# Performance work log

Hardware: AMD Instinct MI355X
Metric: run time of the kernel (lower is better)

## Reference

```python
import jax, jax.numpy as jnp
from jax import lax
import numpy as np

B, T, E, H, V = 64, 512, 256, 256, 50000

def _lstm_dir(xs, Wih, Whh, b, reverse):
    # xs: [T, B, in_dim]; PyTorch gate order i,f,g,o; returns (outputs [T,B,H], final h [B,H])
    def step(carry, xt):
        h, c = carry
        g = xt @ Wih.T + h @ Whh.T + b
        i, f, gg, o = jnp.split(g, 4, axis=-1)
        c = jax.nn.sigmoid(f) * c + jax.nn.sigmoid(i) * jnp.tanh(gg)
        h = jax.nn.sigmoid(o) * jnp.tanh(c)
        return (h, c), h
    z = jnp.zeros((xs.shape[1], Whh.shape[1]), xs.dtype)
    (hT, _), hs = lax.scan(step, (z, z), xs, reverse=reverse)
    return hs, hT

def setup_inputs() -> dict:
    key = jax.random.key(0)
    ks = jax.random.split(key, 20)
    s = 1.0 / np.sqrt(H)
    u = lambda k, sh: jax.random.uniform(k, sh, jnp.float32, -s, s)
    x = jax.random.randint(ks[0], (B, T), 0, V)
    embed = jax.random.normal(ks[1], (V, E), jnp.float32)
    embed = embed.at[0].set(0.0)  # padding_idx=0
    d = {"x": x, "embed": embed}
    i = 2
    for l, in_dim in [(0, E), (1, 2 * H)]:
        for dname in ("f", "b"):
            d[f"Wih_l{l}_{dname}"] = u(ks[i], (4 * H, in_dim)); i += 1
            d[f"Whh_l{l}_{dname}"] = u(ks[i], (4 * H, H)); i += 1
            d[f"b_l{l}_{dname}"] = u(ks[i], (4 * H,)); i += 1  # = b_ih + b_hh fused
    d["Wlin"] = u(ks[i], (1, 2 * H)); d["blin"] = u(ks[i + 1], (1,))
    return d

def reference(x, embed, Wih_l0_f, Whh_l0_f, b_l0_f, Wih_l0_b, Whh_l0_b, b_l0_b,
              Wih_l1_f, Whh_l1_f, b_l1_f, Wih_l1_b, Whh_l1_b, b_l1_b, Wlin, blin):
    xs = embed[x].transpose(1, 0, 2)  # [T, B, E]
    # layer 0
    hf, _ = _lstm_dir(xs, Wih_l0_f, Whh_l0_f, b_l0_f, reverse=False)
    hb, _ = _lstm_dir(xs, Wih_l0_b, Whh_l0_b, b_l0_b, reverse=True)
    xs1 = jnp.concatenate([hf, hb], axis=-1)  # [T, B, 2H]
    # layer 1
    _, hTf = _lstm_dir(xs1, Wih_l1_f, Whh_l1_f, b_l1_f, reverse=False)
    _, hTb = _lstm_dir(xs1, Wih_l1_b, Whh_l1_b, b_l1_b, reverse=True)
    last = jnp.concatenate([hTf, hTb], axis=-1)  # [B, 2H]
    out = last @ Wlin.T + blin  # [B, 1]
    return out[:, 0]
```

## Files before the change

kernel.cpp:

```cpp
#include <hip/hip_runtime.h>
#include <hip/hip_fp16.h>


typedef _Float16 f16;
typedef _Float16 half8 __attribute__((ext_vector_type(8)));
typedef float floatx4 __attribute__((ext_vector_type(4)));

#if __has_builtin(__builtin_amdgcn_global_load_lds)
#define HAS_GLL 1
#endif

#if __has_builtin(__builtin_amdgcn_exp2f)
#define EXP2F __builtin_amdgcn_exp2f
#else
#define EXP2F exp2f
#endif
#if __has_builtin(__builtin_amdgcn_rcpf)
#define RCPF __builtin_amdgcn_rcpf
#else
#define RCPF(x) (1.0f/(x))
#endif

__device__ __forceinline__ float sigf(float x) {
  return RCPF(1.f + EXP2F(-1.4426950408889634f * x));
}
__device__ __forceinline__ float tanhf_(float x) {
  return 2.f * RCPF(1.f + EXP2F(-2.8853900817779268f * x)) - 1.f;
}


__global__ void k_cvt_embed(const float* __restrict__ src, f16* __restrict__ dst, int n8) {
  int i = blockIdx.x * blockDim.x + threadIdx.x;
  if (i >= n8) return;
  const float4* s = (const float4*)(src + (size_t)i * 8);
  float4 a = s[0], b = s[1];
  half8 h = { (f16)a.x,(f16)a.y,(f16)a.z,(f16)a.w,(f16)b.x,(f16)b.y,(f16)b.z,(f16)b.w };
  *(half8*)(dst + (size_t)i * 8) = h;
}

__global__ void k_cvt_wih(const float* __restrict__ sf, const float* __restrict__ sb,
                          f16* __restrict__ dst, int K, int logK, int total) {
  int i = blockIdx.x * blockDim.x + threadIdx.x;
  if (i >= total) return;
  int k = i & (K - 1);
  int n = i >> logK;
  int d = n >> 10;
  int rem = n & 1023;
  int j = rem >> 2, g = rem & 3;
  const float* s = d ? sb : sf;
  dst[i] = (f16)s[(size_t)((g << 8) + j) * K + k];
}

__global__ void k_cvt_whh(const float* __restrict__ sf, const float* __restrict__ sb,
                          f16* __restrict__ dst) {
  int i = blockIdx.x * blockDim.x + threadIdx.x;
  if (i >= 524288) return;
  int d = i >> 18, rem = i & 262143;
  dst[i] = (f16)((d ? sb : sf)[rem]);
}


template<int KD, bool GATHER>
__global__ __launch_bounds__(256)
void k_gemm(const f16* __restrict__ Abase, const f16* __restrict__ Bmat,
            const int* __restrict__ xtok, f16* __restrict__ C) {
  __shared__ __align__(16) char Al[128 * 64 * 2];
  __shared__ __align__(16) char Bl[128 * 64 * 2];
  __shared__ int toks[128];
  const int tid = threadIdx.x;
  const int lane = tid & 63, wave = tid >> 6;
  const int mt = blockIdx.x & 255;
  const int nt = blockIdx.x >> 8;
  const int Mb = mt * 128, Nb = nt * 128;

  if (GATHER) {
    if (tid < 128) {
      int m = Mb + tid;
      toks[tid] = xtok[(m & 63) * 512 + (m >> 6)];
    }
  }
  __syncthreads();

  const f16* asrc[4]; const f16* bsrc[4];
#pragma unroll
  for (int it = 0; it < 4; ++it) {
    int g = it * 256 + tid;
    int row = g >> 3, gc = g & 7;
    if (GATHER) asrc[it] = Abase + (size_t)toks[row] * KD + gc * 8;
    else        asrc[it] = Abase + (size_t)(Mb + row) * KD + gc * 8;
    bsrc[it] = Bmat + (size_t)(Nb + row) * KD + gc * 8;
  }

  floatx4 acc[4][4];
#pragma unroll
  for (int mi = 0; mi < 4; ++mi)
#pragma unroll
    for (int ni = 0; ni < 4; ++ni)
      acc[mi][ni] = (floatx4){0.f, 0.f, 0.f, 0.f};

  const int wr = wave >> 1, wc = wave & 1;

  for (int kt = 0; kt < KD / 64; ++kt) {
    __syncthreads();
#ifdef HAS_GLL
#pragma unroll
    for (int it = 0; it < 4; ++it) {
      __builtin_amdgcn_global_load_lds(
          (const __attribute__((address_space(1))) void*)(asrc[it]),
          (__attribute__((address_space(3))) void*)(Al + (it * 256 + wave * 64) * 16), 16, 0, 0);
      __builtin_amdgcn_global_load_lds(
          (const __attribute__((address_space(1))) void*)(bsrc[it]),
          (__attribute__((address_space(3))) void*)(Bl + (it * 256 + wave * 64) * 16), 16, 0, 0);
      asrc[it] += 64; bsrc[it] += 64;
    }
#else
    uint4 va[4], vb[4];
#pragma unroll
    for (int it = 0; it < 4; ++it) {
      va[it] = *(const uint4*)(asrc[it]);
      vb[it] = *(const uint4*)(bsrc[it]);
      asrc[it] += 64; bsrc[it] += 64;
    }
#pragma unroll
    for (int it = 0; it < 4; ++it) {
      *(uint4*)(Al + (it * 256 + wave * 64) * 16 + lane * 16) = va[it];
      *(uint4*)(Bl + (it * 256 + wave * 64) * 16 + lane * 16) = vb[it];
    }
#endif
    __syncthreads();

#pragma unroll
    for (int kk = 0; kk < 2; ++kk) {
      half8 av[4], bv[4];
#pragma unroll
      for (int mi = 0; mi < 4; ++mi) {
        int row = wr * 64 + mi * 16 + (lane & 15);
        av[mi] = *(const half8*)(Al + row * 128 + kk * 64 + (lane >> 4) * 16);
      }
#pragma unroll
      for (int ni = 0; ni < 4; ++ni) {
        int row = wc * 64 + ni * 16 + (lane & 15);
        bv[ni] = *(const half8*)(Bl + row * 128 + kk * 64 + (lane >> 4) * 16);
      }
#pragma unroll
      for (int mi = 0; mi < 4; ++mi)
#pragma unroll
        for (int ni = 0; ni < 4; ++ni)
          acc[mi][ni] = __builtin_amdgcn_mfma_f32_16x16x32_f16(av[mi], bv[ni], acc[mi][ni], 0, 0, 0);
    }
  }

#pragma unroll
  for (int mi = 0; mi < 4; ++mi) {
#pragma unroll
    for (int ni = 0; ni < 4; ++ni) {
      floatx4 v = acc[mi][ni];
      int n = Nb + wc * 64 + ni * 16 + (lane & 15);
#pragma unroll
      for (int r = 0; r < 4; ++r) {
        int m = Mb + wr * 64 + mi * 16 + (lane >> 4) * 4 + r;
        C[(size_t)m * 2048 + n] = (f16)v[r];
      }
    }
  }
}


template<int LAYER, int OWNBASE>
__device__ __forceinline__ void scan_body(
    const f16* __restrict__ proj, const f16* __restrict__ whh,
    const float* __restrict__ bias_f, const float* __restrict__ bias_b,
    f16* ring, float* __restrict__ finalh, unsigned* __restrict__ ctr,
    char* Hl) {
  constexpr int PEERBASE = 128 - OWNBASE;
  constexpr int BLK = OWNBASE >> 7;
  const int tid = threadIdx.x, lane = tid & 63, wave = tid >> 6;
  const int gid = blockIdx.x & 7;
  const int d = gid & 1, bgrp = gid >> 1;
  const int bbase = bgrp * 16;
  const int rowsel = lane >> 4, l15 = lane & 15;
  const int jlocal = OWNBASE + wave * 16 + l15;
  const int klocal = wave * 16 + l15;
  const int bA = l15;
  unsigned* flagOwn  = ctr + gid * 64 + BLK * 16;
  unsigned* flagPeer = ctr + gid * 64 + (1 - BLK) * 16;

  half8 wreg[4][8];
#pragma unroll
  for (int g = 0; g < 4; ++g)
#pragma unroll
    for (int kk = 0; kk < 8; ++kk)
      wreg[g][kk] = *(const half8*)(whh + ((size_t)(d * 1024 + g * 256 + jlocal)) * 256
                                    + kk * 32 + rowsel * 8);

  const float* bptr = d ? bias_b : bias_f;
  float bias[4];
#pragma unroll
  for (int g = 0; g < 4; ++g) bias[g] = bptr[g * 256 + jlocal];

  *(uint4*)(Hl + tid * 16) = make_uint4(0, 0, 0, 0);
  {
    const int gslot = d ? 513 : 0;
    int zr = tid >> 5, zc = (tid & 31) * 4;
    *(uint2*)(ring + ((size_t)gslot * 64 + bbase + zr) * 512 + d * 256 + OWNBASE + zc) =
        make_uint2(0, 0);
  }
  __syncthreads();
  if (tid == 0)
    __hip_atomic_store(flagOwn, 1u, __ATOMIC_RELEASE, __HIP_MEMORY_SCOPE_AGENT);

  float cst[4] = {0.f, 0.f, 0.f, 0.f};

  uint2 pj[4];
  {
    int t0 = d ? 511 : 0;
#pragma unroll
    for (int r = 0; r < 4; ++r)
      pj[r] = *(const uint2*)(proj + ((size_t)t0 * 64 + bbase + rowsel * 4 + r) * 2048
                              + d * 1024 + (size_t)jlocal * 4);
  }

  for (int s = 0; s < 512; ++s) {
    if (tid == 0) {
      unsigned target = (unsigned)(s + 1);
      unsigned v; int gd = 0;
      do {
        v = __hip_atomic_load(flagPeer, __ATOMIC_RELAXED, __HIP_MEMORY_SCOPE_AGENT);
      } while (v < target && ++gd < (1 << 18));
      (void)__hip_atomic_load(flagPeer, __ATOMIC_ACQUIRE, __HIP_MEMORY_SCOPE_AGENT);
    }
    __syncthreads();

    const int rslot = d ? 513 - s : s;
    uint4 a4p[4];
    {
      const f16* pr = ring + ((size_t)rslot * 64 + bbase + bA) * 512 + d * 256 + PEERBASE
                      + rowsel * 8;
#pragma unroll
      for (int i = 0; i < 4; ++i)
        a4p[i] = *(const uint4*)(pr + i * 32);
    }
    uint2 pjn[4];
    {
      int sn = (s < 511) ? s + 1 : 511;
      int tn = d ? 511 - sn : sn;
#pragma unroll
      for (int r = 0; r < 4; ++r)
        pjn[r] = *(const uint2*)(proj + ((size_t)tn * 64 + bbase + rowsel * 4 + r) * 2048
                                 + d * 1024 + (size_t)jlocal * 4);
    }

    floatx4 acc[4];
#pragma unroll
    for (int r = 0; r < 4; ++r) {
      union { uint2 u; f16 h[4]; } cv; cv.u = pj[r];
      acc[0][r] = (float)cv.h[0] + bias[0];
      acc[1][r] = (float)cv.h[1] + bias[1];
      acc[2][r] = (float)cv.h[2] + bias[2];
      acc[3][r] = (float)cv.h[3] + bias[3];
    }

    {
      const int rb = ((s & 1) ^ 1) * 4096;
      const int swz = (bA & 7) << 4;
#pragma unroll
      for (int i = 0; i < 4; ++i) {
        uint4 a4o = *(const uint4*)(Hl + rb + ((bA * 256 + i * 64 + rowsel * 16) ^ swz));
        half8 av = __builtin_bit_cast(half8, a4o);
#pragma unroll
        for (int g = 0; g < 4; ++g)
          acc[g] = __builtin_amdgcn_mfma_f32_16x16x32_f16(av, wreg[g][(OWNBASE >> 5) + i],
                                                          acc[g], 0, 0, 0);
      }
    }

#pragma unroll
    for (int i = 0; i < 4; ++i) {
      half8 av = __builtin_bit_cast(half8, a4p[i]);
#pragma unroll
      for (int g = 0; g < 4; ++g)
        acc[g] = __builtin_amdgcn_mfma_f32_16x16x32_f16(av, wreg[g][(PEERBASE >> 5) + i],
                                                        acc[g], 0, 0, 0);
    }

    const int wslot = d ? 512 - s : s + 1;
    float hvv[4];
    f16 hhv[4];
#pragma unroll
    for (int r = 0; r < 4; ++r) {
      float iv = sigf(acc[0][r]);
      float fv = sigf(acc[1][r]);
      float gv = tanhf_(acc[2][r]);
      float ov = sigf(acc[3][r]);
      cst[r] = fv * cst[r] + iv * gv;
      hvv[r] = ov * tanhf_(cst[r]);
      hhv[r] = (f16)hvv[r];
    }

    {
      char* wbuf = Hl + (s & 1) * 4096;
#pragma unroll
      for (int r = 0; r < 4; ++r) {
        int row = rowsel * 4 + r;
        *(f16*)(wbuf + ((row * 256 + klocal * 2) ^ ((row & 7) << 4))) = hhv[r];
        ring[((size_t)wslot * 64 + bbase + row) * 512 + d * 256 + jlocal] = hhv[r];
      }
    }
    if (LAYER == 1 && s == 511) {
#pragma unroll
      for (int r = 0; r < 4; ++r)
        finalh[(size_t)(d * 64 + bbase + rowsel * 4 + r) * 256 + jlocal] = hvv[r];
    }

    __syncthreads();
    if (tid == 0)
      __hip_atomic_store(flagOwn, (unsigned)(s + 2), __ATOMIC_RELEASE,
                         __HIP_MEMORY_SCOPE_AGENT);

#pragma unroll
    for (int r = 0; r < 4; ++r) pj[r] = pjn[r];
  }
}

template<int LAYER>
__global__ __launch_bounds__(512, 2)
void k_scan(const f16* __restrict__ proj, const f16* __restrict__ whh,
            const float* __restrict__ bias_f, const float* __restrict__ bias_b,
            f16* ring, float* __restrict__ finalh, unsigned* __restrict__ ctr) {
  __shared__ __align__(16) char Hl[8192];
  if ((blockIdx.x >> 3) == 0)
    scan_body<LAYER, 0>(proj, whh, bias_f, bias_b, ring, finalh, ctr, Hl);
  else
    scan_body<LAYER, 128>(proj, whh, bias_f, bias_b, ring, finalh, ctr, Hl);
}

__global__ void k_final(const float* __restrict__ fh, const float* __restrict__ wlin,
                        const float* __restrict__ blin, float* __restrict__ out) {
  int tid = threadIdx.x;
  int b = tid >> 2, part = tid & 3;
  float sum = 0.f;
#pragma unroll 4
  for (int jj = 0; jj < 128; ++jj) {
    int j = part * 128 + jj;
    float lastv = (j < 256) ? fh[b * 256 + j] : fh[(64 + b) * 256 + (j - 256)];
    sum += lastv * wlin[j];
  }
  sum += __shfl_xor(sum, 1);
  sum += __shfl_xor(sum, 2);
  if (part == 0) out[b] = sum + blin[0];
}

extern "C" void kernel_launch(void* const* d_in, const int* in_sizes, int n_in,
                              void* d_out, int out_size, void* d_ws, size_t ws_size,
                              hipStream_t stream) {
  const int*   x     = (const int*)  d_in[0];
  const float* embed = (const float*)d_in[1];
  const float* wih0f = (const float*)d_in[2];
  const float* whh0f = (const float*)d_in[3];
  const float* b0f   = (const float*)d_in[4];
  const float* wih0b = (const float*)d_in[5];
  const float* whh0b = (const float*)d_in[6];
  const float* b0b   = (const float*)d_in[7];
  const float* wih1f = (const float*)d_in[8];
  const float* whh1f = (const float*)d_in[9];
  const float* b1f   = (const float*)d_in[10];
  const float* wih1b = (const float*)d_in[11];
  const float* whh1b = (const float*)d_in[12];
  const float* b1b   = (const float*)d_in[13];
  const float* wlin  = (const float*)d_in[14];
  const float* blin  = (const float*)d_in[15];

  char* ws = (char*)d_ws;
  size_t off = 0;
  auto alloc = [&](size_t bytes) {
    char* p = ws + off;
    off = (off + bytes + 511) & ~(size_t)511;
    return p;
  };
  f16* embed16 = (f16*)alloc((size_t)50000 * 256 * 2);
  f16* wih0_16 = (f16*)alloc((size_t)2048 * 256 * 2);
  f16* wih1_16 = (f16*)alloc((size_t)2048 * 512 * 2);
  f16* whh0_16 = (f16*)alloc((size_t)2 * 1024 * 256 * 2);
  f16* whh1_16 = (f16*)alloc((size_t)2 * 1024 * 256 * 2);
  f16* proj    = (f16*)alloc((size_t)32768 * 2048 * 2);
  f16* ring    = (f16*)alloc((size_t)514 * 64 * 512 * 2);
  float* fh    = (float*)alloc((size_t)2 * 64 * 256 * 4);
  unsigned* ctr = (unsigned*)alloc((size_t)8 * 64 * 4);

  if (off > ws_size) {
    hipMemsetAsync(d_out, 0, (size_t)out_size * 4, stream);
    return;
  }

  k_cvt_embed<<<(12800000 / 8 + 255) / 256, 256, 0, stream>>>(embed, embed16, 12800000 / 8);
  k_cvt_wih<<<(2048 * 256 + 255) / 256, 256, 0, stream>>>(wih0f, wih0b, wih0_16, 256, 8, 2048 * 256);
  k_cvt_wih<<<(2048 * 512 + 255) / 256, 256, 0, stream>>>(wih1f, wih1b, wih1_16, 512, 9, 2048 * 512);
  k_cvt_whh<<<(524288 + 255) / 256, 256, 0, stream>>>(whh0f, whh0b, whh0_16);
  k_cvt_whh<<<(524288 + 255) / 256, 256, 0, stream>>>(whh1f, whh1b, whh1_16);

  k_gemm<256, true><<<4096, 256, 0, stream>>>(embed16, wih0_16, x, proj);
  hipMemsetAsync(ctr, 0, (size_t)8 * 64 * 4, stream);
  k_scan<0><<<16, 512, 0, stream>>>(proj, whh0_16, b0f, b0b, ring, nullptr, ctr);

  k_gemm<512, false><<<4096, 256, 0, stream>>>(ring + 32768, wih1_16, nullptr, proj);
  hipMemsetAsync(ctr, 0, (size_t)8 * 64 * 4, stream);
  k_scan<1><<<16, 512, 0, stream>>>(proj, whh1_16, b1f, b1b, ring, fh, ctr);

  k_final<<<1, 256, 0, stream>>>(fh, wlin, blin, (float*)d_out);
}
```

Baseline: 3.154 ms.

## Consolidate LSTM scan into four blocks each processing all batch slices

Reduces the recurrent scan grid from 16 blocks to 4. Each block now loops over four 16-row batch slices per timestep, keeping per-slice cell state, projections and a larger LDS hidden buffer. Per-slice flag handshakes with the peer block are kept. This cuts the number of blocks holding recurrent weights in registers, but serialises four slices inside each block per step, lengthening the critical path.

```diff
diff --git a/kernel.cpp b/kernel.cpp
--- a/kernel.cpp
+++ b/kernel.cpp
@@ -173,17 +173,13 @@
     f16* ring, float* __restrict__ finalh, unsigned* __restrict__ ctr,
     char* Hl) {
   constexpr int PEERBASE = 128 - OWNBASE;
-  constexpr int BLK = OWNBASE >> 7;
+  constexpr int JH = OWNBASE >> 7;
   const int tid = threadIdx.x, lane = tid & 63, wave = tid >> 6;
-  const int gid = blockIdx.x & 7;
-  const int d = gid & 1, bgrp = gid >> 1;
-  const int bbase = bgrp * 16;
+  const int d = blockIdx.x & 1;
   const int rowsel = lane >> 4, l15 = lane & 15;
   const int jlocal = OWNBASE + wave * 16 + l15;
   const int klocal = wave * 16 + l15;
   const int bA = l15;
-  unsigned* flagOwn  = ctr + gid * 64 + BLK * 16;
-  unsigned* flagPeer = ctr + gid * 64 + (1 - BLK) * 16;
 
   half8 wreg[4][8];
 #pragma unroll
@@ -198,127 +194,141 @@
 #pragma unroll
   for (int g = 0; g < 4; ++g) bias[g] = bptr[g * 256 + jlocal];
 
-  *(uint4*)(Hl + tid * 16) = make_uint4(0, 0, 0, 0);
+#pragma unroll
+  for (int i = 0; i < 4; ++i)
+    ((uint4*)Hl)[i * 512 + tid] = make_uint4(0, 0, 0, 0);
   {
     const int gslot = d ? 513 : 0;
-    int zr = tid >> 5, zc = (tid & 31) * 4;
-    *(uint2*)(ring + ((size_t)gslot * 64 + bbase + zr) * 512 + d * 256 + OWNBASE + zc) =
-        make_uint2(0, 0);
+    int zr = tid >> 3, zc = (tid & 7) * 8;
+    *(uint4*)(ring + ((size_t)gslot * 64 + zr) * 512 + d * 256 + OWNBASE + zc) =
+        make_uint4(0, 0, 0, 0);
   }
   __syncthreads();
-  if (tid == 0)
-    __hip_atomic_store(flagOwn, 1u, __ATOMIC_RELEASE, __HIP_MEMORY_SCOPE_AGENT);
-
-  float cst[4] = {0.f, 0.f, 0.f, 0.f};
-
-  uint2 pj[4];
+  if (tid == 0) {
+#pragma unroll
+    for (int sl = 0; sl < 4; ++sl)
+      __hip_atomic_store(ctr + (d * 4 + sl) * 64 + JH * 16, 1u,
+                         __ATOMIC_RELEASE, __HIP_MEMORY_SCOPE_AGENT);
+  }
+
+  float cst[4][4] = {};
+
+  uint2 pj[4][4];
   {
     int t0 = d ? 511 : 0;
 #pragma unroll
-    for (int r = 0; r < 4; ++r)
-      pj[r] = *(const uint2*)(proj + ((size_t)t0 * 64 + bbase + rowsel * 4 + r) * 2048
-                              + d * 1024 + (size_t)jlocal * 4);
+    for (int sl = 0; sl < 4; ++sl)
+#pragma unroll
+      for (int r = 0; r < 4; ++r)
+        pj[sl][r] = *(const uint2*)(proj + ((size_t)t0 * 64 + sl * 16 + rowsel * 4 + r) * 2048
+                                    + d * 1024 + (size_t)jlocal * 4);
   }
 
   for (int s = 0; s < 512; ++s) {
-    if (tid == 0) {
-      unsigned target = (unsigned)(s + 1);
-      unsigned v; int gd = 0;
-      do {
-        v = __hip_atomic_load(flagPeer, __ATOMIC_RELAXED, __HIP_MEMORY_SCOPE_AGENT);
-      } while (v < target && ++gd < (1 << 18));
-      (void)__hip_atomic_load(flagPeer, __ATOMIC_ACQUIRE, __HIP_MEMORY_SCOPE_AGENT);
-    }
-    __syncthreads();
-
     const int rslot = d ? 513 - s : s;
-    uint4 a4p[4];
-    {
-      const f16* pr = ring + ((size_t)rslot * 64 + bbase + bA) * 512 + d * 256 + PEERBASE
-                      + rowsel * 8;
-#pragma unroll
-      for (int i = 0; i < 4; ++i)
-        a4p[i] = *(const uint4*)(pr + i * 32);
-    }
-    uint2 pjn[4];
-    {
-      int sn = (s < 511) ? s + 1 : 511;
-      int tn = d ? 511 - sn : sn;
+    const int wslot = d ? 512 - s : s + 1;
+    const int sn = (s < 511) ? s + 1 : 511;
+    const int tn = d ? 511 - sn : sn;
+
+#pragma unroll
+    for (int sl = 0; sl < 4; ++sl) {
+      unsigned* flagOwn  = ctr + (d * 4 + sl) * 64 + JH * 16;
+      unsigned* flagPeer = ctr + (d * 4 + sl) * 64 + (1 - JH) * 16;
+      const int bbase = sl * 16;
+
+      if (tid == 0) {
+        unsigned target = (unsigned)(s + 1);
+        unsigned v; int gd = 0;
+        do {
+          v = __hip_atomic_load(flagPeer, __ATOMIC_RELAXED, __HIP_MEMORY_SCOPE_AGENT);
+        } while (v < target && ++gd < (1 << 18));
+        (void)__hip_atomic_load(flagPeer, __ATOMIC_ACQUIRE, __HIP_MEMORY_SCOPE_AGENT);
+      }
+      __syncthreads();
+
+      uint4 a4p[4];
+      {
+        const f16* pr = ring + ((size_t)rslot * 64 + bbase + bA) * 512 + d * 256 + PEERBASE
+                        + rowsel * 8;
+#pragma unroll
+        for (int i = 0; i < 4; ++i)
+          a4p[i] = *(const uint4*)(pr + i * 32);
+      }
+      uint2 pjn[4];
 #pragma unroll
       for (int r = 0; r < 4; ++r)
         pjn[r] = *(const uint2*)(proj + ((size_t)tn * 64 + bbase + rowsel * 4 + r) * 2048
                                  + d * 1024 + (size_t)jlocal * 4);
-    }
-
-    floatx4 acc[4];
-#pragma unroll
-    for (int r = 0; r < 4; ++r) {
-      union { uint2 u; f16 h[4]; } cv; cv.u = pj[r];
-      acc[0][r] = (float)cv.h[0] + bias[0];
-      acc[1][r] = (float)cv.h[1] + bias[1];
-      acc[2][r] = (float)cv.h[2] + bias[2];
-      acc[3][r] = (float)cv.h[3] + bias[3];
-    }
-
-    {
-      const int rb = ((s & 1) ^ 1) * 4096;
-      const int swz = (bA & 7) << 4;
+
+      floatx4 acc[4];
+#pragma unroll
+      for (int r = 0; r < 4; ++r) {
+        union { uint2 u; f16 h[4]; } cv; cv.u = pj[sl][r];
+        acc[0][r] = (float)cv.h[0] + bias[0];
+        acc[1][r] = (float)cv.h[1] + bias[1];
+        acc[2][r] = (float)cv.h[2] + bias[2];
+        acc[3][r] = (float)cv.h[3] + bias[3];
+      }
+
+      {
+        const char* rb = Hl + sl * 8192 + ((s & 1) ^ 1) * 4096;
+        const int swz = (bA & 7) << 4;
+#pragma unroll
+        for (int i = 0; i < 4; ++i) {
+          uint4 a4o = *(const uint4*)(rb + ((bA * 256 + i * 64 + rowsel * 16) ^ swz));
+          half8 av = __builtin_bit_cast(half8, a4o);
+#pragma unroll
+          for (int g = 0; g < 4; ++g)
+            acc[g] = __builtin_amdgcn_mfma_f32_16x16x32_f16(av, wreg[g][(OWNBASE >> 5) + i],
+                                                            acc[g], 0, 0, 0);
+        }
+      }
+
 #pragma unroll
       for (int i = 0; i < 4; ++i) {
-        uint4 a4o = *(const uint4*)(Hl + rb + ((bA * 256 + i * 64 + rowsel * 16) ^ swz));
-        half8 av = __builtin_bit_cast(half8, a4o);
+        half8 av = __builtin_bit_cast(half8, a4p[i]);
 #pragma unroll
         for (int g = 0; g < 4; ++g)
-          acc[g] = __builtin_amdgcn_mfma_f32_16x16x32_f16(av, wreg[g][(OWNBASE >> 5) + i],
+          acc[g] = __builtin_amdgcn_mfma_f32_16x16x32_f16(av, wreg[g][(PEERBASE >> 5) + i],
                                                           acc[g], 0, 0, 0);
       }
-    }
-
-#pragma unroll
-    for (int i = 0; i < 4; ++i) {
-      half8 av = __builtin_bit_cast(half8, a4p[i]);
-#pragma unroll
-      for (int g = 0; g < 4; ++g)
-        acc[g] = __builtin_amdgcn_mfma_f32_16x16x32_f16(av, wreg[g][(PEERBASE >> 5) + i],
-                                                        acc[g], 0, 0, 0);
-    }
-
-    const int wslot = d ? 512 - s : s + 1;
-    float hvv[4];
-    f16 hhv[4];
-#pragma unroll
-    for (int r = 0; r < 4; ++r) {
-      float iv = sigf(acc[0][r]);
-      float fv = sigf(acc[1][r]);
-      float gv = tanhf_(acc[2][r]);
-      float ov = sigf(acc[3][r]);
-      cst[r] = fv * cst[r] + iv * gv;
-      hvv[r] = ov * tanhf_(cst[r]);
-      hhv[r] = (f16)hvv[r];
-    }
-
-    {
-      char* wbuf = Hl + (s & 1) * 4096;
+
+      float hvv[4];
+      f16 hhv[4];
 #pragma unroll
       for (int r = 0; r < 4; ++r) {
-        int row = rowsel * 4 + r;
-        *(f16*)(wbuf + ((row * 256 + klocal * 2) ^ ((row & 7) << 4))) = hhv[r];
-        ring[((size_t)wslot * 64 + bbase + row) * 512 + d * 256 + jlocal] = hhv[r];
-      }
-    }
-    if (LAYER == 1 && s == 511) {
-#pragma unroll
-      for (int r = 0; r < 4; ++r)
-        finalh[(size_t)(d * 64 + bbase + rowsel * 4 + r) * 256 + jlocal] = hvv[r];
-    }
-
-    __syncthreads();
-    if (tid == 0)
-      __hip_atomic_store(flagOwn, (unsigned)(s + 2), __ATOMIC_RELEASE,
-                         __HIP_MEMORY_SCOPE_AGENT);
-
-#pragma unroll
-    for (int r = 0; r < 4; ++r) pj[r] = pjn[r];
+        float iv = sigf(acc[0][r]);
+        float fv = sigf(acc[1][r]);
+        float gv = tanhf_(acc[2][r]);
+        float ov = sigf(acc[3][r]);
+        cst[sl][r] = fv * cst[sl][r] + iv * gv;
+        hvv[r] = ov * tanhf_(cst[sl][r]);
+        hhv[r] = (f16)hvv[r];
+      }
+
+      {
+        char* wbuf = Hl + sl * 8192 + (s & 1) * 4096;
+#pragma unroll
+        for (int r = 0; r < 4; ++r) {
+          int row = rowsel * 4 + r;
+          *(f16*)(wbuf + ((row * 256 + klocal * 2) ^ ((row & 7) << 4))) = hhv[r];
+          ring[((size_t)wslot * 64 + bbase + row) * 512 + d * 256 + jlocal] = hhv[r];
+        }
+      }
+      if (LAYER == 1 && s == 511) {
+#pragma unroll
+        for (int r = 0; r < 4; ++r)
+          finalh[(size_t)(d * 64 + bbase + rowsel * 4 + r) * 256 + jlocal] = hvv[r];
+      }
+
+      __syncthreads();
+      if (tid == 0)
+        __hip_atomic_store(flagOwn, (unsigned)(s + 2), __ATOMIC_RELEASE,
+                           __HIP_MEMORY_SCOPE_AGENT);
+
+#pragma unroll
+      for (int r = 0; r < 4; ++r) pj[sl][r] = pjn[r];
+    }
   }
 }
 
@@ -327,8 +337,8 @@
 void k_scan(const f16* __restrict__ proj, const f16* __restrict__ whh,
             const float* __restrict__ bias_f, const float* __restrict__ bias_b,
             f16* ring, float* __restrict__ finalh, unsigned* __restrict__ ctr) {
-  __shared__ __align__(16) char Hl[8192];
-  if ((blockIdx.x >> 3) == 0)
+  __shared__ __align__(16) char Hl[32768];
+  if ((blockIdx.x >> 1) == 0)
     scan_body<LAYER, 0>(proj, whh, bias_f, bias_b, ring, finalh, ctr, Hl);
   else
     scan_body<LAYER, 128>(proj, whh, bias_f, bias_b, ring, finalh, ctr, Hl);
@@ -400,11 +410,11 @@
 
   k_gemm<256, true><<<4096, 256, 0, stream>>>(embed16, wih0_16, x, proj);
   hipMemsetAsync(ctr, 0, (size_t)8 * 64 * 4, stream);
-  k_scan<0><<<16, 512, 0, stream>>>(proj, whh0_16, b0f, b0b, ring, nullptr, ctr);
+  k_scan<0><<<4, 512, 0, stream>>>(proj, whh0_16, b0f, b0b, ring, nullptr, ctr);
 
   k_gemm<512, false><<<4096, 256, 0, stream>>>(ring + 32768, wih1_16, nullptr, proj);
   hipMemsetAsync(ctr, 0, (size_t)8 * 64 * 4, stream);
-  k_scan<1><<<16, 512, 0, stream>>>(proj, whh1_16, b1f, b1b, ring, fh, ctr);
+  k_scan<1><<<4, 512, 0, stream>>>(proj, whh1_16, b1f, b1b, ring, fh, ctr);
 
   k_final<<<1, 256, 0, stream>>>(fh, wlin, blin, (float*)d_out);
 }
```

After: 11.65 ms. +269.4%, slower.
